# Kernel tuning notes

Hardware: AMD Instinct MI355X
Metric: run time of the kernel (lower is better)

Reference implementation:

```python
import jax, jax.numpy as jnp
import numpy as np

N_NODES = 17   # fixed by Linear(256, 17) + residual add
D = 512        # feature dim
H = 8          # number of attention heads


def setup_inputs() -> dict:
    key = jax.random.key(0)
    ks = jax.random.split(key, 8)
    return {
        "Xs": jax.random.normal(ks[0], (N_NODES, D), dtype=jnp.float32),
        "ROIs_b": jax.random.uniform(ks[1], (N_NODES, 3), dtype=jnp.float32),
        "adj": jnp.zeros((N_NODES, N_NODES), dtype=jnp.float32),  # unused in forward
        "FC": jax.random.normal(ks[2], (H, D, D), dtype=jnp.float32) * (1.414 / np.sqrt(D)),
        "W1": jax.random.normal(ks[3], (H, D + 3, 256), dtype=jnp.float32) * (1.0 / np.sqrt(D + 3)),
        "b1": jnp.zeros((H, 256), dtype=jnp.float32),
        "W2": jax.random.normal(ks[4], (H, 256, N_NODES), dtype=jnp.float32) * (1.0 / np.sqrt(256)),
        "b2": jnp.zeros((H, N_NODES), dtype=jnp.float32),
        "conv_w": jax.random.normal(ks[5], (H,), dtype=jnp.float32) * 0.3,
        "conv_b": jnp.zeros((1,), dtype=jnp.float32),
    }


def reference(Xs, ROIs_b, adj, FC, W1, b1, W2, b2, conv_w, conv_b):
    # All 8 heads batched over leading axis h (original launches them as
    # separate Python-level modules).
    # f_input = relu(Xs @ FC) per head: [H, N, D]
    f = jax.nn.relu(jnp.einsum('nd,hde->hne', Xs, FC))
    # concat coordinates: [H, N, D+3]
    coords = jnp.broadcast_to(ROIs_b[None], (f.shape[0], ROIs_b.shape[0], ROIs_b.shape[1]))
    cat = jnp.concatenate([f, coords], axis=-1)
    # 2-layer MLP: Linear(515,256) -> tanh -> Linear(256,17): [H, N, 17]
    hdn = jnp.tanh(jnp.einsum('hnc,hcm->hnm', cat, W1) + b1[:, None, :])
    att = jnp.einsum('hnm,hmk->hnk', hdn, W2) + b2[:, None, :]
    # permute(1,0) then softmax over dim=1 (the N axis): [H, 17, N]
    att = jax.nn.softmax(jnp.swapaxes(att, 1, 2), axis=-1)
    # weighted sum over nodes: [H, 17, D]
    h_prime = jnp.einsum('hkn,hnd->hkd', att, f)
    # Conv1d(8,1,1) over head axis + ReLU, then residual
    out = jax.nn.relu(jnp.einsum('h,hkd->kd', conv_w, h_prime) + conv_b[0])
    Xs_out = out + Xs  # [17, 512]
    # original returns a list of per-landmark views [1,512,1,1,1]; we return
    # the equivalent stacked array plus passthrough ROIs
    return Xs_out, ROIs_b
```

## Files before the change

kernel.cpp:

```cpp
#include <hip/hip_runtime.h>

#define NN 17
#define D  512
#define H  8
#define C1 515
#define M  256

#define XPAD 20
#define RSN  36
#define RSG  (NN * RSN)
#define SMEM_FL (32 * RSG)

__device__ __forceinline__ void fma4(float4& a, float x, const float4& w) {
    a.x = fmaf(x, w.x, a.x); a.y = fmaf(x, w.y, a.y);
    a.z = fmaf(x, w.z, a.z); a.w = fmaf(x, w.w, a.w);
}

__global__ __launch_bounds__(256) void k1_f(const float* __restrict__ Xs,
                                            const float* __restrict__ FC,
                                            float* __restrict__ f) {
    const int b = blockIdx.x;
    const int et = b & 15, h = b >> 4;
    const int t = threadIdx.x, tw = t & 7, cg = t >> 3;
    __shared__ float sm[SMEM_FL];
    for (int i = t; i < NN * D; i += 256) {
        const int n = i >> 9, d = i & 511;
        sm[d * XPAD + n] = Xs[i];
    }
    __syncthreads();
    float4 acc[NN];
#pragma unroll
    for (int n = 0; n < NN; ++n) acc[n] = make_float4(0.f, 0.f, 0.f, 0.f);
    const float4* fc4 = (const float4*)(FC + (size_t)h * D * D) + et * 8 + tw;
#pragma unroll 4
    for (int i = 0; i < 16; ++i) {
        const int d = cg + (i << 5);
        const float4 w = fc4[d << 7];
        const float* xr = sm + d * XPAD;
#pragma unroll
        for (int n4 = 0; n4 < 4; ++n4) {
            const float4 x = *(const float4*)(xr + (n4 << 2));
            fma4(acc[n4 * 4 + 0], x.x, w);
            fma4(acc[n4 * 4 + 1], x.y, w);
            fma4(acc[n4 * 4 + 2], x.z, w);
            fma4(acc[n4 * 4 + 3], x.w, w);
        }
        fma4(acc[16], xr[16], w);
    }
    __syncthreads();
    float* rr = sm + cg * RSG + tw * 4;
#pragma unroll
    for (int n = 0; n < NN; ++n) *(float4*)(rr + n * RSN) = acc[n];
    __syncthreads();
    for (int i = t; i < NN * 32; i += 256) {
        const int n = i >> 5, e = i & 31;
        float s = 0.f;
#pragma unroll 8
        for (int g = 0; g < 32; ++g) s += sm[g * RSG + n * RSN + e];
        f[((h * NN + n) << 9) + (et << 5) + e] = fmaxf(s, 0.f);
    }
}

__global__ __launch_bounds__(256) void k2_hdn(const float* __restrict__ f,
                                              const float* __restrict__ ROIs,
                                              const float* __restrict__ W1,
                                              const float* __restrict__ b1,
                                              float* __restrict__ hdn) {
    const int b = blockIdx.x;
    const int mt = b & 7, h = b >> 3;
    const int t = threadIdx.x, tw = t & 7, cg = t >> 3;
    __shared__ float sm[SMEM_FL];
    for (int i = t; i < NN * D; i += 256) {
        const int n = i >> 9, d = i & 511;
        sm[d * XPAD + n] = f[((size_t)(h * NN) << 9) + i];
    }
    if (t < NN * 3) {
        const int n = t / 3, cc = t % 3;
        sm[(D + cc) * XPAD + n] = ROIs[t];
    }
    __syncthreads();
    float4 acc[NN];
#pragma unroll
    for (int n = 0; n < NN; ++n) acc[n] = make_float4(0.f, 0.f, 0.f, 0.f);
    const float4* w4 = (const float4*)(W1 + (size_t)h * C1 * M) + mt * 8 + tw;
#pragma unroll 4
    for (int i = 0; i < 16; ++i) {
        const int c = cg + (i << 5);
        const float4 w = w4[c << 6];
        const float* xr = sm + c * XPAD;
#pragma unroll
        for (int n4 = 0; n4 < 4; ++n4) {
            const float4 x = *(const float4*)(xr + (n4 << 2));
            fma4(acc[n4 * 4 + 0], x.x, w);
            fma4(acc[n4 * 4 + 1], x.y, w);
            fma4(acc[n4 * 4 + 2], x.z, w);
            fma4(acc[n4 * 4 + 3], x.w, w);
        }
        fma4(acc[16], xr[16], w);
    }
    if (cg < 3) {
        const int c = D + cg;
        const float4 w = w4[c << 6];
        const float* xr = sm + c * XPAD;
#pragma unroll
        for (int n4 = 0; n4 < 4; ++n4) {
            const float4 x = *(const float4*)(xr + (n4 << 2));
            fma4(acc[n4 * 4 + 0], x.x, w);
            fma4(acc[n4 * 4 + 1], x.y, w);
            fma4(acc[n4 * 4 + 2], x.z, w);
            fma4(acc[n4 * 4 + 3], x.w, w);
        }
        fma4(acc[16], xr[16], w);
    }
    __syncthreads();
    float* rr = sm + cg * RSG + tw * 4;
#pragma unroll
    for (int n = 0; n < NN; ++n) *(float4*)(rr + n * RSN) = acc[n];
    __syncthreads();
    for (int i = t; i < NN * 32; i += 256) {
        const int n = i >> 5, m = i & 31;
        float s = b1[h * M + (mt << 5) + m];
#pragma unroll 8
        for (int g = 0; g < 32; ++g) s += sm[g * RSG + n * RSN + m];
        hdn[(h * NN + n) * M + (mt << 5) + m] = tanhf(s);
    }
}

__global__ __launch_bounds__(256) void k34(const float* __restrict__ hdn,
                                           const float* __restrict__ W2,
                                           const float* __restrict__ b2,
                                           const float* __restrict__ f,
                                           const float* __restrict__ conv_w,
                                           const float* __restrict__ conv_b,
                                           const float* __restrict__ Xs,
                                           const float* __restrict__ ROIs,
                                           float* __restrict__ out) {
    const int k = blockIdx.x, t = threadIdx.x;
    __shared__ float swk[H][M + 4];
    __shared__ float sa[H][NN];
    __shared__ float cw[H];
    for (int i = t; i < H * M; i += 256) {
        const int h = i >> 8, m = i & 255;
        swk[h][m] = W2[(size_t)(h * M + m) * NN + k];
    }
    if (t < H) cw[t] = conv_w[t];
    __syncthreads();
    if (t < H * NN) {
        const int h = t / NN, n = t % NN;
        const float4* a4 = (const float4*)(hdn + (h * NN + n) * M);
        const float4* w4 = (const float4*)(&swk[h][0]);
        float acc = b2[h * NN + k];
#pragma unroll 8
        for (int m4 = 0; m4 < M / 4; ++m4) {
            const float4 av = a4[m4];
            const float4 wv = w4[m4];
            acc = fmaf(av.x, wv.x, acc); acc = fmaf(av.y, wv.y, acc);
            acc = fmaf(av.z, wv.z, acc); acc = fmaf(av.w, wv.w, acc);
        }
        sa[h][n] = acc;
    }
    __syncthreads();
    if (t < H) {
        float mx = -1e30f;
#pragma unroll
        for (int n = 0; n < NN; ++n) mx = fmaxf(mx, sa[t][n]);
        float e[NN];
        float s = 0.f;
#pragma unroll
        for (int n = 0; n < NN; ++n) { e[n] = __expf(sa[t][n] - mx); s += e[n]; }
        const float inv = 1.f / s;
#pragma unroll
        for (int n = 0; n < NN; ++n) sa[t][n] = e[n] * inv;
    }
    __syncthreads();
    const float cb = conv_b[0];
    float acc0 = 0.f, acc1 = 0.f;
    for (int h = 0; h < H; ++h) {
        float w0 = 0.f, w1 = 0.f;
#pragma unroll
        for (int n = 0; n < NN; ++n) {
            const float a = sa[h][n];
            const float* fr = f + (size_t)((h * NN + n) << 9);
            w0 = fmaf(a, fr[t], w0);
            w1 = fmaf(a, fr[t + 256], w1);
        }
        acc0 = fmaf(cw[h], w0, acc0);
        acc1 = fmaf(cw[h], w1, acc1);
    }
    out[(k << 9) + t]       = fmaxf(acc0 + cb, 0.f) + Xs[(k << 9) + t];
    out[(k << 9) + t + 256] = fmaxf(acc1 + cb, 0.f) + Xs[(k << 9) + t + 256];
    if (k == 0 && t < NN * 3) out[NN * D + t] = ROIs[t];
}

extern "C" void kernel_launch(void* const* d_in, const int* in_sizes, int n_in,
                              void* d_out, int out_size, void* d_ws, size_t ws_size,
                              hipStream_t stream) {
    const float* Xs     = (const float*)d_in[0];
    const float* ROIs   = (const float*)d_in[1];
    const float* FC     = (const float*)d_in[3];
    const float* W1     = (const float*)d_in[4];
    const float* b1     = (const float*)d_in[5];
    const float* W2     = (const float*)d_in[6];
    const float* b2     = (const float*)d_in[7];
    const float* conv_w = (const float*)d_in[8];
    const float* conv_b = (const float*)d_in[9];
    float* out = (float*)d_out;

    float* f   = (float*)d_ws;
    float* hdn = f + H * NN * D;

    k1_f  <<<H * 16, 256, 0, stream>>>(Xs, FC, f);
    k2_hdn<<<H * 8,  256, 0, stream>>>(f, ROIs, W1, b1, hdn);
    k34   <<<NN,     256, 0, stream>>>(hdn, W2, b2, f, conv_w, conv_b, Xs, ROIs, out);
}
```

Baseline: 107.3 us.

## Fuse three kernels into one cooperative kernel with grid-wide syncs

Merges the three stage kernels (FC projection, MLP hidden layer, attention/softmax/aggregation) into a single cooperative launch of 128 blocks. Grid-wide barriers separate the stages, replacing the two kernel launch boundaries. The aim is to cut launch overhead and inter-kernel gaps. In exchange it adds cooperative-launch overhead and grid-sync cost, and blocks sit idle during the later stages.

New measurement: 159.1 us. 1.48x slower.

```diff
diff --git a/kernel.cpp b/kernel.cpp
--- a/kernel.cpp
+++ b/kernel.cpp
@@ -1,4 +1,7 @@
 #include <hip/hip_runtime.h>
+#include <hip/hip_cooperative_groups.h>
+
+namespace cg = cooperative_groups;
 
 #define NN 17
 #define D  512
@@ -16,180 +19,176 @@
     a.z = fmaf(x, w.z, a.z); a.w = fmaf(x, w.w, a.w);
 }
 
-__global__ __launch_bounds__(256) void k1_f(const float* __restrict__ Xs,
-                                            const float* __restrict__ FC,
-                                            float* __restrict__ f) {
-    const int b = blockIdx.x;
-    const int et = b & 15, h = b >> 4;
-    const int t = threadIdx.x, tw = t & 7, cg = t >> 3;
-    __shared__ float sm[SMEM_FL];
-    for (int i = t; i < NN * D; i += 256) {
-        const int n = i >> 9, d = i & 511;
-        sm[d * XPAD + n] = Xs[i];
+__global__ __launch_bounds__(256) void fused_all(
+        const float* __restrict__ Xs, const float* __restrict__ ROIs,
+        const float* __restrict__ FC, const float* __restrict__ W1,
+        const float* __restrict__ b1, const float* __restrict__ W2,
+        const float* __restrict__ b2, const float* __restrict__ conv_w,
+        const float* __restrict__ conv_b, float* __restrict__ f,
+        float* __restrict__ hdn, float* __restrict__ out) {
+    cg::grid_group grid = cg::this_grid();
+    __shared__ __align__(16) float sm[SMEM_FL];
+    const int b = blockIdx.x, t = threadIdx.x;
+
+    {
+        const int et = b & 15, h = b >> 4;
+        const int tw = t & 7, cgp = t >> 3;
+        for (int i = t; i < NN * D; i += 256) {
+            const int n = i >> 9, d = i & 511;
+            sm[d * XPAD + n] = Xs[i];
+        }
+        __syncthreads();
+        float4 acc[NN];
+#pragma unroll
+        for (int n = 0; n < NN; ++n) acc[n] = make_float4(0.f, 0.f, 0.f, 0.f);
+        const float4* fc4 = (const float4*)(FC + (size_t)h * D * D) + et * 8 + tw;
+#pragma unroll 4
+        for (int i = 0; i < 16; ++i) {
+            const int d = cgp + (i << 5);
+            const float4 w = fc4[d << 7];
+            const float* xr = sm + d * XPAD;
+#pragma unroll
+            for (int n4 = 0; n4 < 4; ++n4) {
+                const float4 x = *(const float4*)(xr + (n4 << 2));
+                fma4(acc[n4 * 4 + 0], x.x, w);
+                fma4(acc[n4 * 4 + 1], x.y, w);
+                fma4(acc[n4 * 4 + 2], x.z, w);
+                fma4(acc[n4 * 4 + 3], x.w, w);
+            }
+            fma4(acc[16], xr[16], w);
+        }
+        __syncthreads();
+        float* rr = sm + cgp * RSG + tw * 4;
+#pragma unroll
+        for (int n = 0; n < NN; ++n) *(float4*)(rr + n * RSN) = acc[n];
+        __syncthreads();
+        for (int i = t; i < NN * 32; i += 256) {
+            const int n = i >> 5, e = i & 31;
+            float s = 0.f;
+#pragma unroll 8
+            for (int g = 0; g < 32; ++g) s += sm[g * RSG + n * RSN + e];
+            f[((h * NN + n) << 9) + (et << 5) + e] = fmaxf(s, 0.f);
+        }
     }
-    __syncthreads();
-    float4 acc[NN];
-#pragma unroll
-    for (int n = 0; n < NN; ++n) acc[n] = make_float4(0.f, 0.f, 0.f, 0.f);
-    const float4* fc4 = (const float4*)(FC + (size_t)h * D * D) + et * 8 + tw;
+    grid.sync();
+
+    if (b < 64) {
+        const int mt = b & 7, h = b >> 3;
+        const int tw = t & 7, cgp = t >> 3;
+        for (int i = t; i < NN * D; i += 256) {
+            const int n = i >> 9, d = i & 511;
+            sm[d * XPAD + n] = f[((size_t)(h * NN) << 9) + i];
+        }
+        if (t < NN * 3) {
+            const int n = t / 3, cc = t % 3;
+            sm[(D + cc) * XPAD + n] = ROIs[t];
+        }
+        __syncthreads();
+        float4 acc[NN];
+#pragma unroll
+        for (int n = 0; n < NN; ++n) acc[n] = make_float4(0.f, 0.f, 0.f, 0.f);
+        const float4* w4 = (const float4*)(W1 + (size_t)h * C1 * M) + mt * 8 + tw;
 #pragma unroll 4
-    for (int i = 0; i < 16; ++i) {
-        const int d = cg + (i << 5);
-        const float4 w = fc4[d << 7];
-        const float* xr = sm + d * XPAD;
-#pragma unroll
-        for (int n4 = 0; n4 < 4; ++n4) {
-            const float4 x = *(const float4*)(xr + (n4 << 2));
-            fma4(acc[n4 * 4 + 0], x.x, w);
-            fma4(acc[n4 * 4 + 1], x.y, w);
-            fma4(acc[n4 * 4 + 2], x.z, w);
-            fma4(acc[n4 * 4 + 3], x.w, w);
-        }
-        fma4(acc[16], xr[16], w);
+        for (int i = 0; i < 16; ++i) {
+            const int c = cgp + (i << 5);
+            const float4 w = w4[c << 6];
+            const float* xr = sm + c * XPAD;
+#pragma unroll
+            for (int n4 = 0; n4 < 4; ++n4) {
+                const float4 x = *(const float4*)(xr + (n4 << 2));
+                fma4(acc[n4 * 4 + 0], x.x, w);
+                fma4(acc[n4 * 4 + 1], x.y, w);
+                fma4(acc[n4 * 4 + 2], x.z, w);
+                fma4(acc[n4 * 4 + 3], x.w, w);
+            }
+            fma4(acc[16], xr[16], w);
+        }
+        if (cgp < 3) {
+            const int c = D + cgp;
+            const float4 w = w4[c << 6];
+            const float* xr = sm + c * XPAD;
+#pragma unroll
+            for (int n4 = 0; n4 < 4; ++n4) {
+                const float4 x = *(const float4*)(xr + (n4 << 2));
+                fma4(acc[n4 * 4 + 0], x.x, w);
+                fma4(acc[n4 * 4 + 1], x.y, w);
+                fma4(acc[n4 * 4 + 2], x.z, w);
+                fma4(acc[n4 * 4 + 3], x.w, w);
+            }
+            fma4(acc[16], xr[16], w);
+        }
+        __syncthreads();
+        float* rr = sm + cgp * RSG + tw * 4;
+#pragma unroll
+        for (int n = 0; n < NN; ++n) *(float4*)(rr + n * RSN) = acc[n];
+        __syncthreads();
+        for (int i = t; i < NN * 32; i += 256) {
+            const int n = i >> 5, m = i & 31;
+            float s = b1[h * M + (mt << 5) + m];
+#pragma unroll 8
+            for (int g = 0; g < 32; ++g) s += sm[g * RSG + n * RSN + m];
+            hdn[(h * NN + n) * M + (mt << 5) + m] = tanhf(s);
+        }
     }
-    __syncthreads();
-    float* rr = sm + cg * RSG + tw * 4;
-#pragma unroll
-    for (int n = 0; n < NN; ++n) *(float4*)(rr + n * RSN) = acc[n];
-    __syncthreads();
-    for (int i = t; i < NN * 32; i += 256) {
-        const int n = i >> 5, e = i & 31;
-        float s = 0.f;
+    grid.sync();
+
+    if (b < NN) {
+        const int k = b;
+        float* swk = sm;
+        float* sa  = sm + H * (M + 4);
+        float* cw  = sa + H * NN;
+        for (int i = t; i < H * M; i += 256) {
+            const int h = i >> 8, m = i & 255;
+            swk[h * (M + 4) + m] = W2[(size_t)(h * M + m) * NN + k];
+        }
+        if (t < H) cw[t] = conv_w[t];
+        __syncthreads();
+        if (t < H * NN) {
+            const int h = t / NN, n = t % NN;
+            const float4* a4 = (const float4*)(hdn + (h * NN + n) * M);
+            const float4* w4 = (const float4*)(swk + h * (M + 4));
+            float acc = b2[h * NN + k];
 #pragma unroll 8
-        for (int g = 0; g < 32; ++g) s += sm[g * RSG + n * RSN + e];
-        f[((h * NN + n) << 9) + (et << 5) + e] = fmaxf(s, 0.f);
+            for (int m4 = 0; m4 < M / 4; ++m4) {
+                const float4 av = a4[m4];
+                const float4 wv = w4[m4];
+                acc = fmaf(av.x, wv.x, acc); acc = fmaf(av.y, wv.y, acc);
+                acc = fmaf(av.z, wv.z, acc); acc = fmaf(av.w, wv.w, acc);
+            }
+            sa[h * NN + n] = acc;
+        }
+        __syncthreads();
+        if (t < H) {
+            float mx = -1e30f;
+#pragma unroll
+            for (int n = 0; n < NN; ++n) mx = fmaxf(mx, sa[t * NN + n]);
+            float e[NN];
+            float s = 0.f;
+#pragma unroll
+            for (int n = 0; n < NN; ++n) { e[n] = __expf(sa[t * NN + n] - mx); s += e[n]; }
+            const float inv = 1.f / s;
+#pragma unroll
+            for (int n = 0; n < NN; ++n) sa[t * NN + n] = e[n] * inv;
+        }
+        __syncthreads();
+        const float cb = conv_b[0];
+        float acc0 = 0.f, acc1 = 0.f;
+        for (int h = 0; h < H; ++h) {
+            float w0 = 0.f, w1 = 0.f;
+#pragma unroll
+            for (int n = 0; n < NN; ++n) {
+                const float a = sa[h * NN + n];
+                const float* fr = f + (size_t)((h * NN + n) << 9);
+                w0 = fmaf(a, fr[t], w0);
+                w1 = fmaf(a, fr[t + 256], w1);
+            }
+            acc0 = fmaf(cw[h], w0, acc0);
+            acc1 = fmaf(cw[h], w1, acc1);
+        }
+        out[(k << 9) + t]       = fmaxf(acc0 + cb, 0.f) + Xs[(k << 9) + t];
+        out[(k << 9) + t + 256] = fmaxf(acc1 + cb, 0.f) + Xs[(k << 9) + t + 256];
+        if (k == 0 && t < NN * 3) out[NN * D + t] = ROIs[t];
     }
-}
-
-__global__ __launch_bounds__(256) void k2_hdn(const float* __restrict__ f,
-                                              const float* __restrict__ ROIs,
-                                              const float* __restrict__ W1,
-                                              const float* __restrict__ b1,
-                                              float* __restrict__ hdn) {
-    const int b = blockIdx.x;
-    const int mt = b & 7, h = b >> 3;
-    const int t = threadIdx.x, tw = t & 7, cg = t >> 3;
-    __shared__ float sm[SMEM_FL];
-    for (int i = t; i < NN * D; i += 256) {
-        const int n = i >> 9, d = i & 511;
-        sm[d * XPAD + n] = f[((size_t)(h * NN) << 9) + i];
-    }
-    if (t < NN * 3) {
-        const int n = t / 3, cc = t % 3;
-        sm[(D + cc) * XPAD + n] = ROIs[t];
-    }
-    __syncthreads();
-    float4 acc[NN];
-#pragma unroll
-    for (int n = 0; n < NN; ++n) acc[n] = make_float4(0.f, 0.f, 0.f, 0.f);
-    const float4* w4 = (const float4*)(W1 + (size_t)h * C1 * M) + mt * 8 + tw;
-#pragma unroll 4
-    for (int i = 0; i < 16; ++i) {
-        const int c = cg + (i << 5);
-        const float4 w = w4[c << 6];
-        const float* xr = sm + c * XPAD;
-#pragma unroll
-        for (int n4 = 0; n4 < 4; ++n4) {
-            const float4 x = *(const float4*)(xr + (n4 << 2));
-            fma4(acc[n4 * 4 + 0], x.x, w);
-            fma4(acc[n4 * 4 + 1], x.y, w);
-            fma4(acc[n4 * 4 + 2], x.z, w);
-            fma4(acc[n4 * 4 + 3], x.w, w);
-        }
-        fma4(acc[16], xr[16], w);
-    }
-    if (cg < 3) {
-        const int c = D + cg;
-        const float4 w = w4[c << 6];
-        const float* xr = sm + c * XPAD;
-#pragma unroll
-        for (int n4 = 0; n4 < 4; ++n4) {
-            const float4 x = *(const float4*)(xr + (n4 << 2));
-            fma4(acc[n4 * 4 + 0], x.x, w);
-            fma4(acc[n4 * 4 + 1], x.y, w);
-            fma4(acc[n4 * 4 + 2], x.z, w);
-            fma4(acc[n4 * 4 + 3], x.w, w);
-        }
-        fma4(acc[16], xr[16], w);
-    }
-    __syncthreads();
-    float* rr = sm + cg * RSG + tw * 4;
-#pragma unroll
-    for (int n = 0; n < NN; ++n) *(float4*)(rr + n * RSN) = acc[n];
-    __syncthreads();
-    for (int i = t; i < NN * 32; i += 256) {
-        const int n = i >> 5, m = i & 31;
-        float s = b1[h * M + (mt << 5) + m];
-#pragma unroll 8
-        for (int g = 0; g < 32; ++g) s += sm[g * RSG + n * RSN + m];
-        hdn[(h * NN + n) * M + (mt << 5) + m] = tanhf(s);
-    }
-}
-
-__global__ __launch_bounds__(256) void k34(const float* __restrict__ hdn,
-                                           const float* __restrict__ W2,
-                                           const float* __restrict__ b2,
-                                           const float* __restrict__ f,
-                                           const float* __restrict__ conv_w,
-                                           const float* __restrict__ conv_b,
-                                           const float* __restrict__ Xs,
-                                           const float* __restrict__ ROIs,
-                                           float* __restrict__ out) {
-    const int k = blockIdx.x, t = threadIdx.x;
-    __shared__ float swk[H][M + 4];
-    __shared__ float sa[H][NN];
-    __shared__ float cw[H];
-    for (int i = t; i < H * M; i += 256) {
-        const int h = i >> 8, m = i & 255;
-        swk[h][m] = W2[(size_t)(h * M + m) * NN + k];
-    }
-    if (t < H) cw[t] = conv_w[t];
-    __syncthreads();
-    if (t < H * NN) {
-        const int h = t / NN, n = t % NN;
-        const float4* a4 = (const float4*)(hdn + (h * NN + n) * M);
-        const float4* w4 = (const float4*)(&swk[h][0]);
-        float acc = b2[h * NN + k];
-#pragma unroll 8
-        for (int m4 = 0; m4 < M / 4; ++m4) {
-            const float4 av = a4[m4];
-            const float4 wv = w4[m4];
-            acc = fmaf(av.x, wv.x, acc); acc = fmaf(av.y, wv.y, acc);
-            acc = fmaf(av.z, wv.z, acc); acc = fmaf(av.w, wv.w, acc);
-        }
-        sa[h][n] = acc;
-    }
-    __syncthreads();
-    if (t < H) {
-        float mx = -1e30f;
-#pragma unroll
-        for (int n = 0; n < NN; ++n) mx = fmaxf(mx, sa[t][n]);
-        float e[NN];
-        float s = 0.f;
-#pragma unroll
-        for (int n = 0; n < NN; ++n) { e[n] = __expf(sa[t][n] - mx); s += e[n]; }
-        const float inv = 1.f / s;
-#pragma unroll
-        for (int n = 0; n < NN; ++n) sa[t][n] = e[n] * inv;
-    }
-    __syncthreads();
-    const float cb = conv_b[0];
-    float acc0 = 0.f, acc1 = 0.f;
-    for (int h = 0; h < H; ++h) {
-        float w0 = 0.f, w1 = 0.f;
-#pragma unroll
-        for (int n = 0; n < NN; ++n) {
-            const float a = sa[h][n];
-            const float* fr = f + (size_t)((h * NN + n) << 9);
-            w0 = fmaf(a, fr[t], w0);
-            w1 = fmaf(a, fr[t + 256], w1);
-        }
-        acc0 = fmaf(cw[h], w0, acc0);
-        acc1 = fmaf(cw[h], w1, acc1);
-    }
-    out[(k << 9) + t]       = fmaxf(acc0 + cb, 0.f) + Xs[(k << 9) + t];
-    out[(k << 9) + t + 256] = fmaxf(acc1 + cb, 0.f) + Xs[(k << 9) + t + 256];
-    if (k == 0 && t < NN * 3) out[NN * D + t] = ROIs[t];
 }
 
 extern "C" void kernel_launch(void* const* d_in, const int* in_sizes, int n_in,
@@ -209,7 +208,9 @@
     float* f   = (float*)d_ws;
     float* hdn = f + H * NN * D;
 
-    k1_f  <<<H * 16, 256, 0, stream>>>(Xs, FC, f);
-    k2_hdn<<<H * 8,  256, 0, stream>>>(f, ROIs, W1, b1, hdn);
-    k34   <<<NN,     256, 0, stream>>>(hdn, W2, b2, f, conv_w, conv_b, Xs, ROIs, out);
+    void* args[] = {(void*)&Xs, (void*)&ROIs, (void*)&FC, (void*)&W1, (void*)&b1,
+                    (void*)&W2, (void*)&b2, (void*)&conv_w, (void*)&conv_b,
+                    (void*)&f, (void*)&hdn, (void*)&out};
+    hipLaunchCooperativeKernel(reinterpret_cast<void*>(&fused_all),
+                               dim3(128), dim3(256), args, 0, stream);
 }
```
